# Kernel tuning notes

Measured on AMD Instinct MI355X. Metric: run time of the kernel, lower is better.

## Reference

```python
import jax, jax.numpy as jnp
import numpy as np

B, N, PATCH_SIZE = 32, 131072, 64
L = N // PATCH_SIZE


def setup_inputs() -> dict:
    key = jax.random.key(0)
    k_pts, k_perm = jax.random.split(key)
    pts = jax.random.normal(k_pts, (B, N, 3), dtype=jnp.float32)
    # serialization order: a permutation of the B*N flattened point indices
    # (stands in for the hilbert-curve order produced by Point.serialization)
    orders = jax.random.permutation(k_perm, B * N).astype(jnp.int64)
    return {"pts": pts, "orders": orders}


def reference(pts, orders):
    # gather-reorder by serialization order: pts.flatten(0,1)[orders]
    reordered = pts.reshape(B * N, 3)[orders].reshape(B, N, 3)
    # split into patches along the point dim: [B, L, P, 3]
    patches = reordered.reshape(B, L, PATCH_SIZE, 3)
    # virtual_center=True path: per-patch mean
    centers = patches.mean(axis=2)                      # [B, L, 3]
    patches = patches - centers[:, :, None, :]          # center-subtract
    return (patches, centers)
```

## Files before the change

kernel.cpp:

```cpp
#include <hip/hip_runtime.h>


#define PD_B 32
#define PD_N 131072
#define PD_PATCH 64
#define PD_L (PD_N / PD_PATCH)
#define PD_NPATCH (PD_B * PD_L)
#define PPW 4

struct pt3 { float x, y, z; };

__global__ __launch_bounds__(256) void PatchDivider_57621281243393_kernel(
    const float* __restrict__ pts,
    const int* __restrict__ orders,
    float* __restrict__ out)
{
    const int gtid = blockIdx.x * blockDim.x + threadIdx.x;
    const int wid  = gtid >> 6;
    const int lane = threadIdx.x & 63;
    const int patch0 = wid * PPW;

    int idx[PPW];
    #pragma unroll
    for (int k = 0; k < PPW; ++k)
        idx[k] = orders[(patch0 + k) * PD_PATCH + lane];

    pt3 q[PPW];
    #pragma unroll
    for (int k = 0; k < PPW; ++k)
        q[k] = *(const pt3*)(pts + (size_t)idx[k] * 3);

    const float inv = 1.0f / (float)PD_PATCH;

    #pragma unroll
    for (int k = 0; k < PPW; ++k) {
        float sx = q[k].x, sy = q[k].y, sz = q[k].z;
        #pragma unroll
        for (int off = 32; off >= 1; off >>= 1) {
            sx += __shfl_xor(sx, off, 64);
            sy += __shfl_xor(sy, off, 64);
            sz += __shfl_xor(sz, off, 64);
        }
        const float cx = sx * inv;
        const float cy = sy * inv;
        const float cz = sz * inv;

        const int point = (patch0 + k) * PD_PATCH + lane;
        pt3 r = { q[k].x - cx, q[k].y - cy, q[k].z - cz };
        *(pt3*)(out + (size_t)point * 3) = r;

        if (lane == 0) {
            pt3 c = { cx, cy, cz };
            *(pt3*)(out + (size_t)PD_NPATCH * PD_PATCH * 3
                        + (size_t)(patch0 + k) * 3) = c;
        }
    }
}

extern "C" void kernel_launch(void* const* d_in, const int* in_sizes, int n_in,
                              void* d_out, int out_size, void* d_ws, size_t ws_size,
                              hipStream_t stream) {
    const float* pts  = (const float*)d_in[0];
    const int* orders = (const int*)d_in[1];
    float* out        = (float*)d_out;

    const int waves = PD_NPATCH / PPW;
    const int block = 256;
    const int grid  = waves * 64 / block;

    PatchDivider_57621281243393_kernel<<<grid, block, 0, stream>>>(pts, orders, out);
}
```

Baseline: 92.45 us.

## Restructure gather into windowed per-thread chunks with XCD-aware block mapping

Each thread now handles 8 consecutive output points, loading orders with int4 and writing outputs as contiguous float2 stores, with the patch sum reduced over 8 lanes instead of 64. Gathers are issued in 32 source-index windows so that all blocks touch the same region of pts at roughly the same time, which is meant to improve L2/MALL locality for the random gather. Blocks are mapped round-robin to XCDs so each XCD owns a contiguous output slice. The window loop serializes loads behind data-dependent branches, which may reduce memory-level parallelism.

Result: slower. 99.26 us (+7.4%).

```diff
diff --git a/kernel.cpp b/kernel.cpp
--- a/kernel.cpp
+++ b/kernel.cpp
@@ -1,59 +1,77 @@
 #include <hip/hip_runtime.h>
 
 
-#define PD_B 32
-#define PD_N 131072
-#define PD_PATCH 64
-#define PD_L (PD_N / PD_PATCH)
-#define PD_NPATCH (PD_B * PD_L)
-#define PPW 4
+#define PD_TOTAL  (32 * 131072)
+#define PD_PATCH  64
+#define PD_NPATCH (PD_TOTAL / PD_PATCH)
+#define NXCD      8
+#define PER_XCD   (PD_TOTAL / NXCD)
+#define NBLK      2048
+#define BPX       (NBLK / NXCD)
+#define CHUNK     2048
+#define PPT       8
+#define NW        32
+#define WSHIFT    17
 
-struct pt3 { float x, y, z; };
-
-__global__ __launch_bounds__(256) void PatchDivider_57621281243393_kernel(
+__global__ __launch_bounds__(256, 8) void pd_window(
     const float* __restrict__ pts,
     const int* __restrict__ orders,
     float* __restrict__ out)
 {
-    const int gtid = blockIdx.x * blockDim.x + threadIdx.x;
-    const int wid  = gtid >> 6;
-    const int lane = threadIdx.x & 63;
-    const int patch0 = wid * PPW;
+    const int bid = blockIdx.x;
+    const int xcd = bid & 7;
+    const int blk = bid >> 3;
+    const int t   = threadIdx.x;
+    const int dst0 = xcd * PER_XCD + blk * CHUNK + t * PPT;
 
-    int idx[PPW];
+    int src[PPT];
+    const int4 s0 = *(const int4*)(orders + dst0);
+    const int4 s1 = *(const int4*)(orders + dst0 + 4);
+    src[0] = s0.x; src[1] = s0.y; src[2] = s0.z; src[3] = s0.w;
+    src[4] = s1.x; src[5] = s1.y; src[6] = s1.z; src[7] = s1.w;
+
+    float qx[PPT], qy[PPT], qz[PPT];
+
+    for (int w = 0; w < NW; ++w) {
+        #pragma unroll
+        for (int j = 0; j < PPT; ++j) {
+            if ((src[j] >> WSHIFT) == w) {
+                const float* p = pts + (size_t)src[j] * 3;
+                qx[j] = p[0];
+                qy[j] = p[1];
+                qz[j] = p[2];
+            }
+        }
+    }
+
+    float sx = 0.f, sy = 0.f, sz = 0.f;
     #pragma unroll
-    for (int k = 0; k < PPW; ++k)
-        idx[k] = orders[(patch0 + k) * PD_PATCH + lane];
-
-    pt3 q[PPW];
+    for (int j = 0; j < PPT; ++j) { sx += qx[j]; sy += qy[j]; sz += qz[j]; }
     #pragma unroll
-    for (int k = 0; k < PPW; ++k)
-        q[k] = *(const pt3*)(pts + (size_t)idx[k] * 3);
-
+    for (int off = 1; off <= 4; off <<= 1) {
+        sx += __shfl_xor(sx, off, 64);
+        sy += __shfl_xor(sy, off, 64);
+        sz += __shfl_xor(sz, off, 64);
+    }
     const float inv = 1.0f / (float)PD_PATCH;
+    const float cx = sx * inv, cy = sy * inv, cz = sz * inv;
 
     #pragma unroll
-    for (int k = 0; k < PPW; ++k) {
-        float sx = q[k].x, sy = q[k].y, sz = q[k].z;
-        #pragma unroll
-        for (int off = 32; off >= 1; off >>= 1) {
-            sx += __shfl_xor(sx, off, 64);
-            sy += __shfl_xor(sy, off, 64);
-            sz += __shfl_xor(sz, off, 64);
-        }
-        const float cx = sx * inv;
-        const float cy = sy * inv;
-        const float cz = sz * inv;
+    for (int j = 0; j < PPT; ++j) { qx[j] -= cx; qy[j] -= cy; qz[j] -= cz; }
 
-        const int point = (patch0 + k) * PD_PATCH + lane;
-        pt3 r = { q[k].x - cx, q[k].y - cy, q[k].z - cz };
-        *(pt3*)(out + (size_t)point * 3) = r;
+    float* po = out + (size_t)dst0 * 3;
+    float2* po2 = (float2*)po;
+    #pragma unroll
+    for (int j = 0; j < PPT; j += 2) {
+        po2[0] = make_float2(qx[j],     qy[j]);
+        po2[1] = make_float2(qz[j],     qx[j + 1]);
+        po2[2] = make_float2(qy[j + 1], qz[j + 1]);
+        po2 += 3;
+    }
 
-        if (lane == 0) {
-            pt3 c = { cx, cy, cz };
-            *(pt3*)(out + (size_t)PD_NPATCH * PD_PATCH * 3
-                        + (size_t)(patch0 + k) * 3) = c;
-        }
+    if ((t & 7) == 0) {
+        float* co = out + (size_t)PD_TOTAL * 3 + (size_t)(dst0 >> 6) * 3;
+        co[0] = cx; co[1] = cy; co[2] = cz;
     }
 }
 
@@ -64,9 +82,5 @@
     const int* orders = (const int*)d_in[1];
     float* out        = (float*)d_out;
 
-    const int waves = PD_NPATCH / PPW;
-    const int block = 256;
-    const int grid  = waves * 64 / block;
-
-    PatchDivider_57621281243393_kernel<<<grid, block, 0, stream>>>(pts, orders, out);
+    pd_window<<<NBLK, 256, 0, stream>>>(pts, orders, out);
 }
```

## Bucket-sort gather indices in shared memory before fetching points

Applied to the files above, without the earlier changes.

Each block now takes a 4096-point chunk and bins its order indices into 64 buckets by high bits using a shared-memory histogram and scan. It then issues the point gathers in bucketed order, so nearby source addresses are fetched together, and scatters the results into a shared buffer at their destination slots. Patch means and center subtraction are computed from shared memory and written out coalesced. The aim is better DRAM/cache locality for the random gather, paid for with extra shared memory (about 70KB per block), atomics, several barriers and lower occupancy.

New measurement: 95.48 us. 3.3% more time.

```diff
diff --git a/kernel.cpp b/kernel.cpp
--- a/kernel.cpp
+++ b/kernel.cpp
@@ -1,58 +1,98 @@
 #include <hip/hip_runtime.h>
 
 
-#define PD_B 32
-#define PD_N 131072
-#define PD_PATCH 64
-#define PD_L (PD_N / PD_PATCH)
-#define PD_NPATCH (PD_B * PD_L)
-#define PPW 4
+#define PD_TOTAL  (32 * 131072)
+#define PD_PATCH  64
+#define CHUNK     4096
+#define NBLK      (PD_TOTAL / CHUNK)
+#define PPT       16
+#define NBIN      64
+#define BSHIFT    16
 
 struct pt3 { float x, y, z; };
 
-__global__ __launch_bounds__(256) void PatchDivider_57621281243393_kernel(
+__global__ __launch_bounds__(256, 2) void pd_sorted(
     const float* __restrict__ pts,
     const int* __restrict__ orders,
     float* __restrict__ out)
 {
-    const int gtid = blockIdx.x * blockDim.x + threadIdx.x;
-    const int wid  = gtid >> 6;
-    const int lane = threadIdx.x & 63;
-    const int patch0 = wid * PPW;
+    __shared__ unsigned       ssrc[CHUNK];
+    __shared__ unsigned short sdl [CHUNK];
+    __shared__ float          res [CHUNK * 3];
+    __shared__ int hist[NBIN];
+    __shared__ int bincur[NBIN];
 
-    int idx[PPW];
+    const int t    = threadIdx.x;
+    const int base = blockIdx.x * CHUNK;
+
+    if (t < NBIN) hist[t] = 0;
+    __syncthreads();
+
+    unsigned src[PPT];
     #pragma unroll
-    for (int k = 0; k < PPW; ++k)
-        idx[k] = orders[(patch0 + k) * PD_PATCH + lane];
+    for (int j = 0; j < PPT; ++j) {
+        src[j] = (unsigned)orders[base + t + j * 256];
+        atomicAdd(&hist[src[j] >> BSHIFT], 1);
+    }
+    __syncthreads();
 
-    pt3 q[PPW];
-    #pragma unroll
-    for (int k = 0; k < PPW; ++k)
-        q[k] = *(const pt3*)(pts + (size_t)idx[k] * 3);
-
-    const float inv = 1.0f / (float)PD_PATCH;
+    if (t < NBIN) {
+        const int v = hist[t];
+        int incl = v;
+        #pragma unroll
+        for (int off = 1; off < NBIN; off <<= 1) {
+            const int n = __shfl_up(incl, off, 64);
+            if (t >= off) incl += n;
+        }
+        bincur[t] = incl - v;
+    }
+    __syncthreads();
 
     #pragma unroll
-    for (int k = 0; k < PPW; ++k) {
-        float sx = q[k].x, sy = q[k].y, sz = q[k].z;
+    for (int j = 0; j < PPT; ++j) {
+        const int pos = atomicAdd(&bincur[src[j] >> BSHIFT], 1);
+        ssrc[pos] = src[j];
+        sdl [pos] = (unsigned short)(t + j * 256);
+    }
+    __syncthreads();
+
+    #pragma unroll
+    for (int j = 0; j < PPT; ++j) {
+        const int i = j * 256 + t;
+        const unsigned s  = ssrc[i];
+        const unsigned dl = sdl[i];
+        const pt3 q = *(const pt3*)(pts + (size_t)s * 3);
+        res[dl * 3 + 0] = q.x;
+        res[dl * 3 + 1] = q.y;
+        res[dl * 3 + 2] = q.z;
+    }
+    __syncthreads();
+
+    const int w = t >> 6, lane = t & 63;
+    const float inv = 1.0f / (float)PD_PATCH;
+    for (int p = w; p < 64; p += 4) {
+        const int li = (p * 64 + lane) * 3;
+        const float x = res[li + 0];
+        const float y = res[li + 1];
+        const float z = res[li + 2];
+        float sx = x, sy = y, sz = z;
         #pragma unroll
         for (int off = 32; off >= 1; off >>= 1) {
             sx += __shfl_xor(sx, off, 64);
             sy += __shfl_xor(sy, off, 64);
             sz += __shfl_xor(sz, off, 64);
         }
-        const float cx = sx * inv;
-        const float cy = sy * inv;
-        const float cz = sz * inv;
+        const float cx = sx * inv, cy = sy * inv, cz = sz * inv;
 
-        const int point = (patch0 + k) * PD_PATCH + lane;
-        pt3 r = { q[k].x - cx, q[k].y - cy, q[k].z - cz };
-        *(pt3*)(out + (size_t)point * 3) = r;
+        float* po = out + ((size_t)base + p * 64 + lane) * 3;
+        pt3 r = { x - cx, y - cy, z - cz };
+        *(pt3*)po = r;
 
         if (lane == 0) {
+            float* co = out + (size_t)PD_TOTAL * 3
+                            + ((size_t)blockIdx.x * 64 + p) * 3;
             pt3 c = { cx, cy, cz };
-            *(pt3*)(out + (size_t)PD_NPATCH * PD_PATCH * 3
-                        + (size_t)(patch0 + k) * 3) = c;
+            *(pt3*)co = c;
         }
     }
 }
@@ -64,9 +104,5 @@
     const int* orders = (const int*)d_in[1];
     float* out        = (float*)d_out;
 
-    const int waves = PD_NPATCH / PPW;
-    const int block = 256;
-    const int grid  = waves * 64 / block;
-
-    PatchDivider_57621281243393_kernel<<<grid, block, 0, stream>>>(pts, orders, out);
+    pd_sorted<<<NBLK, 256, 0, stream>>>(pts, orders, out);
 }
```

## Replace random gather with inverse-permutation scatter through workspace buffer

Applied to the files above, without the earlier changes.

Splits the single gather kernel into three passes: build the inverse permutation, scatter points to their reordered positions using coalesced reads, then compute patch centers and subtract them from a contiguous buffer. The aim is to swap random 12-byte gathers for coalesced reads plus random scatter writes. It adds two extra kernel launches, roughly 64 MB of extra workspace traffic, and random 4-byte writes for the inverse. It falls back to a simple gather kernel when the workspace is too small.

Result: slower. 137.5 us (+48.7%).

```diff
diff --git a/kernel.cpp b/kernel.cpp
--- a/kernel.cpp
+++ b/kernel.cpp
@@ -1,59 +1,94 @@
 #include <hip/hip_runtime.h>
 
 
-#define PD_B 32
-#define PD_N 131072
-#define PD_PATCH 64
-#define PD_L (PD_N / PD_PATCH)
-#define PD_NPATCH (PD_B * PD_L)
-#define PPW 4
+#define PD_TOTAL  (32 * 131072)
+#define PD_PATCH  64
+#define PD_NPATCH (PD_TOTAL / PD_PATCH)
+
+#define WS_INV_OFF 0
+#define WS_RAW_OFF ((size_t)PD_TOTAL * 4)
+#define WS_NEEDED  (WS_RAW_OFF + (size_t)PD_TOTAL * 12)
 
 struct pt3 { float x, y, z; };
 
-__global__ __launch_bounds__(256) void PatchDivider_57621281243393_kernel(
-    const float* __restrict__ pts,
-    const int* __restrict__ orders,
+__global__ __launch_bounds__(256) void pd_inv(
+    const int* __restrict__ orders, int* __restrict__ inv)
+{
+    const int i0 = (blockIdx.x * 256 + threadIdx.x) * 4;
+    const int4 s = *(const int4*)(orders + i0);
+    inv[s.x] = i0;
+    inv[s.y] = i0 + 1;
+    inv[s.z] = i0 + 2;
+    inv[s.w] = i0 + 3;
+}
+
+__global__ __launch_bounds__(256) void pd_scatter(
+    const float* __restrict__ pts, const int* __restrict__ inv,
+    float* __restrict__ raw)
+{
+    const int base = blockIdx.x * 1024;
+    #pragma unroll
+    for (int k = 0; k < 4; ++k) {
+        const int s = base + threadIdx.x + k * 256;
+        const pt3 q = *(const pt3*)(pts + (size_t)s * 3);
+        const int d = inv[s];
+        *(pt3*)(raw + (size_t)d * 3) = q;
+    }
+}
+
+__global__ __launch_bounds__(256) void pd_finish(
+    const float* __restrict__ raw, float* __restrict__ out)
+{
+    const int gtid = blockIdx.x * blockDim.x + threadIdx.x;
+    const int wave = gtid >> 6;
+    const int lane = threadIdx.x & 63;
+    const size_t point = (size_t)wave * PD_PATCH + lane;
+
+    const pt3 q = *(const pt3*)(raw + point * 3);
+
+    float sx = q.x, sy = q.y, sz = q.z;
+    #pragma unroll
+    for (int off = 32; off >= 1; off >>= 1) {
+        sx += __shfl_xor(sx, off, 64);
+        sy += __shfl_xor(sy, off, 64);
+        sz += __shfl_xor(sz, off, 64);
+    }
+    const float inv64 = 1.0f / (float)PD_PATCH;
+    const float cx = sx * inv64, cy = sy * inv64, cz = sz * inv64;
+
+    pt3 r = { q.x - cx, q.y - cy, q.z - cz };
+    *(pt3*)(out + point * 3) = r;
+
+    if (lane == 0) {
+        pt3 c = { cx, cy, cz };
+        *(pt3*)(out + (size_t)PD_TOTAL * 3 + (size_t)wave * 3) = c;
+    }
+}
+
+__global__ __launch_bounds__(256) void pd_simple(
+    const float* __restrict__ pts, const int* __restrict__ orders,
     float* __restrict__ out)
 {
     const int gtid = blockIdx.x * blockDim.x + threadIdx.x;
-    const int wid  = gtid >> 6;
+    const int wave = gtid >> 6;
     const int lane = threadIdx.x & 63;
-    const int patch0 = wid * PPW;
-
-    int idx[PPW];
+    const long long point = (long long)wave * PD_PATCH + lane;
+    const int idx = orders[point];
+    const pt3 q = *(const pt3*)(pts + (size_t)idx * 3);
+    float sx = q.x, sy = q.y, sz = q.z;
     #pragma unroll
-    for (int k = 0; k < PPW; ++k)
-        idx[k] = orders[(patch0 + k) * PD_PATCH + lane];
-
-    pt3 q[PPW];
-    #pragma unroll
-    for (int k = 0; k < PPW; ++k)
-        q[k] = *(const pt3*)(pts + (size_t)idx[k] * 3);
-
-    const float inv = 1.0f / (float)PD_PATCH;
-
-    #pragma unroll
-    for (int k = 0; k < PPW; ++k) {
-        float sx = q[k].x, sy = q[k].y, sz = q[k].z;
-        #pragma unroll
-        for (int off = 32; off >= 1; off >>= 1) {
-            sx += __shfl_xor(sx, off, 64);
-            sy += __shfl_xor(sy, off, 64);
-            sz += __shfl_xor(sz, off, 64);
-        }
-        const float cx = sx * inv;
-        const float cy = sy * inv;
-        const float cz = sz * inv;
-
-        const int point = (patch0 + k) * PD_PATCH + lane;
-        pt3 r = { q[k].x - cx, q[k].y - cy, q[k].z - cz };
-        *(pt3*)(out + (size_t)point * 3) = r;
-
-        if (lane == 0) {
-            pt3 c = { cx, cy, cz };
-            *(pt3*)(out + (size_t)PD_NPATCH * PD_PATCH * 3
-                        + (size_t)(patch0 + k) * 3) = c;
-        }
+    for (int off = 32; off >= 1; off >>= 1) {
+        sx += __shfl_xor(sx, off, 64);
+        sy += __shfl_xor(sy, off, 64);
+        sz += __shfl_xor(sz, off, 64);
+    }
+    const float inv64 = 1.0f / (float)PD_PATCH;
+    const float cx = sx * inv64, cy = sy * inv64, cz = sz * inv64;
+    pt3 r = { q.x - cx, q.y - cy, q.z - cz };
+    *(pt3*)(out + point * 3) = r;
+    if (lane == 0) {
+        pt3 c = { cx, cy, cz };
+        *(pt3*)(out + (size_t)PD_TOTAL * 3 + (size_t)wave * 3) = c;
     }
 }
 
@@ -64,9 +99,15 @@
     const int* orders = (const int*)d_in[1];
     float* out        = (float*)d_out;
 
-    const int waves = PD_NPATCH / PPW;
-    const int block = 256;
-    const int grid  = waves * 64 / block;
+    if (ws_size < WS_NEEDED) {
+        pd_simple<<<PD_TOTAL / 256, 256, 0, stream>>>(pts, orders, out);
+        return;
+    }
 
-    PatchDivider_57621281243393_kernel<<<grid, block, 0, stream>>>(pts, orders, out);
+    int*   inv = (int*)((char*)d_ws + WS_INV_OFF);
+    float* raw = (float*)((char*)d_ws + WS_RAW_OFF);
+
+    pd_inv    <<<PD_TOTAL / 1024, 256, 0, stream>>>(orders, inv);
+    pd_scatter<<<PD_TOTAL / 1024, 256, 0, stream>>>(pts, inv, raw);
+    pd_finish <<<PD_TOTAL / 64 / 256 * 64, 256, 0, stream>>>(raw, out);
 }
```
